# Kernel tuning notes

Measured on AMD Instinct MI355X. Metric: run time of the kernel, lower is better.

## Reference

```python
import jax, jax.numpy as jnp
import numpy as np

H = W = 128          # input_size
N = 128              # output_size[0] == output_size[1]
B = 64
LIN = (H - 2) * (W - 2)          # 15876
TRI = (N * N + N) // 2           # 8256
TI, TJ = np.triu_indices(N)
TI = jnp.asarray(TI); TJ = jnp.asarray(TJ)


def setup_inputs() -> dict:
    key = jax.random.key(0)
    ks = jax.random.split(key, 7)
    return {
        "x": jax.random.normal(ks[0], (B, 1, H, W), jnp.float32),
        "conv1_w": jax.random.normal(ks[1], (4, 1, 3, 3), jnp.float32) * 0.1,
        "conv1_b": jax.random.normal(ks[2], (4,), jnp.float32) * 0.1,
        "conv2_w": jax.random.normal(ks[3], (1, 4, 1, 1), jnp.float32) * 0.1,
        "conv2_b": jax.random.normal(ks[4], (1,), jnp.float32) * 0.1,
        "out_w": jax.random.normal(ks[5], (TRI, LIN), jnp.float32) * (1.0 / np.sqrt(LIN)),
        "out_b": jax.random.normal(ks[6], (TRI,), jnp.float32) * 0.01,
    }


def reference(x, conv1_w, conv1_b, conv2_w, conv2_b, out_w, out_b):
    dn = ('NCHW', 'OIHW', 'NCHW')
    # conv1 (1->4, 3x3, VALID) + relu
    h = jax.lax.conv_general_dilated(x, conv1_w, (1, 1), 'VALID', dimension_numbers=dn)
    h = jax.nn.relu(h + conv1_b[None, :, None, None])
    # conv2 (4->1, 1x1)
    h = jax.lax.conv_general_dilated(h, conv2_w, (1, 1), 'VALID', dimension_numbers=dn)
    h = h + conv2_b[None, :, None, None]
    # flatten -> linear
    h = h.reshape(x.shape[0], -1)                       # [B, LIN]
    v = h @ out_w.T + out_b                             # [B, TRI]
    # vectorized symmetric triu scatter (replaces per-sample Python loop)
    y = jnp.zeros((x.shape[0], N, N), v.dtype)
    y = y.at[:, TI, TJ].set(v).at[:, TJ, TI].set(v)
    return y[:, None, :, :]                             # [B, 1, N, N]
```

## Files before the change

### kernel.cpp

```cpp
#include <hip/hip_runtime.h>
#include <hip/hip_bf16.h>

#define H_IN   128
#define W_IN   128
#define B_SZ   64
#define CONV_O 126
#define K_DIM  15876
#define N_TRI  8256
#define N_OUT  128
#define BK     32
#define BN     32
#define NSTEPS 497
#define HPAD   15904
#define KSPLIT 8

typedef short  short8  __attribute__((ext_vector_type(8)));
typedef float  floatx4 __attribute__((ext_vector_type(4)));

__device__ inline short f2bf(float f) {
    union { __hip_bfloat16 h; short s; } u;
    u.h = __float2bfloat16(f);
    return u.s;
}

__global__ __launch_bounds__(256) void conv_kernel(
    const float* __restrict__ x,
    const float* __restrict__ w1,
    const float* __restrict__ b1,
    const float* __restrict__ w2,
    const float* __restrict__ b2,
    unsigned short* __restrict__ h)
{
    int t = blockIdx.x * 256 + threadIdx.x;
    int b = t / HPAD;
    int p = t - b * HPAD;
    float val = 0.f;
    if (p < K_DIM) {
        int oy = p / CONV_O;
        int ox = p - oy * CONV_O;
        const float* xb = x + b * (H_IN * W_IN) + oy * W_IN + ox;
        float xin[9];
#pragma unroll
        for (int dy = 0; dy < 3; ++dy)
#pragma unroll
            for (int dx = 0; dx < 3; ++dx)
                xin[dy * 3 + dx] = xb[dy * W_IN + dx];
        float acc = b2[0];
#pragma unroll
        for (int c = 0; c < 4; ++c) {
            float s = b1[c];
#pragma unroll
            for (int q = 0; q < 9; ++q) s = fmaf(w1[c * 9 + q], xin[q], s);
            s = fmaxf(s, 0.f);
            acc = fmaf(w2[c], s, acc);
        }
        val = acc;
    }
    h[t] = (unsigned short)f2bf(val);
}

__global__ __launch_bounds__(256, 4) void gemm_kernel(
    const unsigned short* __restrict__ h,
    const float* __restrict__ w,
    float* __restrict__ v)
{
    __shared__ __align__(16) short As[64 * 40];
    __shared__ __align__(16) short Bs[32 * 40];

    const int n0    = blockIdx.x * BN;
    const int split = blockIdx.y;
    const int s0 = (NSTEPS * split) / KSPLIT;
    const int s1 = (NSTEPS * (split + 1)) / KSPLIT;

    const int t    = threadIdx.x;
    const int lane = t & 63;
    const int wv   = t >> 6;
    const int quad = lane >> 4;
    const int l16  = lane & 15;

    const int arow = t >> 2, acol = (t & 3) * 8;
    const int brow = t >> 3, bcol = (t & 7) * 4;

    const int mh = (wv >> 1) * 32;
    const int nw = (wv & 1) * 16;

    const int aoff0 = (mh + l16) * 40 + quad * 8;
    const int aoff1 = (mh + 16 + l16) * 40 + quad * 8;
    const int boff  = (nw + l16) * 40 + quad * 8;

    floatx4 acc0 = {0.f, 0.f, 0.f, 0.f};
    floatx4 acc1 = {0.f, 0.f, 0.f, 0.f};

    for (int s = s0; s < s1; ++s) {
        const int k0 = s * BK;

        __syncthreads();
        {
            int4 av = *(const int4*)(h + (size_t)arow * HPAD + k0 + acol);
            *(int4*)(As + arow * 40 + acol) = av;
        }
        {
            const float* wp = w + (size_t)(n0 + brow) * K_DIM + k0 + bcol;
            float4 bv;
            if (k0 + BK <= K_DIM) {
                bv = *(const float4*)wp;
            } else {
                bv.x = (k0 + bcol + 0 < K_DIM) ? wp[0] : 0.f;
                bv.y = (k0 + bcol + 1 < K_DIM) ? wp[1] : 0.f;
                bv.z = (k0 + bcol + 2 < K_DIM) ? wp[2] : 0.f;
                bv.w = (k0 + bcol + 3 < K_DIM) ? wp[3] : 0.f;
            }
            short4 bs = make_short4(f2bf(bv.x), f2bf(bv.y), f2bf(bv.z), f2bf(bv.w));
            *(short4*)(Bs + brow * 40 + bcol) = bs;
        }
        __syncthreads();

        short8 af0 = *(const short8*)(As + aoff0);
        short8 af1 = *(const short8*)(As + aoff1);
        short8 bf  = *(const short8*)(Bs + boff);
        acc0 = __builtin_amdgcn_mfma_f32_16x16x32_bf16(af0, bf, acc0, 0, 0, 0);
        acc1 = __builtin_amdgcn_mfma_f32_16x16x32_bf16(af1, bf, acc1, 0, 0, 0);
    }

    const int n = n0 + nw + l16;
#pragma unroll
    for (int r = 0; r < 4; ++r) {
        int m0 = mh + quad * 4 + r;
        atomicAdd(&v[(size_t)m0 * N_TRI + n], acc0[r]);
        atomicAdd(&v[(size_t)(m0 + 16) * N_TRI + n], acc1[r]);
    }
}

__global__ __launch_bounds__(256) void scatter_kernel(
    const float* __restrict__ v,
    const float* __restrict__ out_b,
    float* __restrict__ y)
{
    int t = blockIdx.x * 256 + threadIdx.x;
    int b  = t >> 14;
    int ij = t & 16383;
    int i = ij >> 7, j = ij & 127;
    int ii = min(i, j), jj = max(i, j);
    int tri = ii * N_OUT - ((ii * (ii - 1)) >> 1) + (jj - ii);
    y[t] = v[(size_t)b * N_TRI + tri] + out_b[tri];
}

extern "C" void kernel_launch(void* const* d_in, const int* in_sizes, int n_in,
                              void* d_out, int out_size, void* d_ws, size_t ws_size,
                              hipStream_t stream) {
    const float* x   = (const float*)d_in[0];
    const float* c1w = (const float*)d_in[1];
    const float* c1b = (const float*)d_in[2];
    const float* c2w = (const float*)d_in[3];
    const float* c2b = (const float*)d_in[4];
    const float* ow  = (const float*)d_in[5];
    const float* ob  = (const float*)d_in[6];
    float* y = (float*)d_out;

    unsigned short* h = (unsigned short*)d_ws;
    float* v = (float*)((char*)d_ws + (size_t)B_SZ * HPAD * 2);

    hipMemsetAsync(v, 0, (size_t)B_SZ * N_TRI * sizeof(float), stream);

    conv_kernel<<<(B_SZ * HPAD) / 256, 256, 0, stream>>>(x, c1w, c1b, c2w, c2b, h);
    gemm_kernel<<<dim3(N_TRI / BN, KSPLIT), 256, 0, stream>>>(h, ow, v);
    scatter_kernel<<<(B_SZ * N_OUT * N_OUT) / 256, 256, 0, stream>>>(v, ob, y);
}
```

Measured before the change: 807.7 us.

## Swizzle activations into MFMA fragment layout and widen GEMM N tile

The conv kernel now writes its bf16 output in a k8-major, fragment-friendly layout, so the GEMM loads A fragments straight from global memory and no longer stages A through LDS. The N tile grows from 32 to 64 with four MFMAs per step, and the K split rises from 8 to 16 for more blocks. Each thread also loads its 8 weights before the barrier. The aim is to cut LDS traffic and per-step overhead and to overlap the weight loads better, at the cost of more atomic adds and repeated global reads of A across blocks.

```diff
diff --git a/kernel.cpp b/kernel.cpp
--- a/kernel.cpp
+++ b/kernel.cpp
@@ -9,10 +9,10 @@
 #define N_TRI  8256
 #define N_OUT  128
 #define BK     32
-#define BN     32
+#define BN     64
 #define NSTEPS 497
-#define HPAD   15904
-#define KSPLIT 8
+#define K8     1988
+#define KSPLIT 16
 
 typedef short  short8  __attribute__((ext_vector_type(8)));
 typedef float  floatx4 __attribute__((ext_vector_type(4)));
@@ -29,16 +29,18 @@
     const float* __restrict__ b1,
     const float* __restrict__ w2,
     const float* __restrict__ b2,
-    unsigned short* __restrict__ h)
+    unsigned short* __restrict__ hsw)
 {
     int t = blockIdx.x * 256 + threadIdx.x;
-    int b = t / HPAD;
-    int p = t - b * HPAD;
+    int j  = t & 7;
+    int m  = (t >> 3) & 63;
+    int k8 = t >> 9;
+    int p  = k8 * 8 + j;
     float val = 0.f;
     if (p < K_DIM) {
         int oy = p / CONV_O;
         int ox = p - oy * CONV_O;
-        const float* xb = x + b * (H_IN * W_IN) + oy * W_IN + ox;
+        const float* xb = x + m * (H_IN * W_IN) + oy * W_IN + ox;
         float xin[9];
 #pragma unroll
         for (int dy = 0; dy < 3; ++dy)
@@ -56,16 +58,15 @@
         }
         val = acc;
     }
-    h[t] = (unsigned short)f2bf(val);
+    hsw[t] = (unsigned short)f2bf(val);
 }
 
 __global__ __launch_bounds__(256, 4) void gemm_kernel(
-    const unsigned short* __restrict__ h,
+    const unsigned short* __restrict__ hsw,
     const float* __restrict__ w,
     float* __restrict__ v)
 {
-    __shared__ __align__(16) short As[64 * 40];
-    __shared__ __align__(16) short Bs[32 * 40];
+    __shared__ __align__(16) short Bs[64 * 40];
 
     const int n0    = blockIdx.x * BN;
     const int split = blockIdx.y;
@@ -78,56 +79,61 @@
     const int quad = lane >> 4;
     const int l16  = lane & 15;
 
-    const int arow = t >> 2, acol = (t & 3) * 8;
-    const int brow = t >> 3, bcol = (t & 7) * 4;
+    const int mh = (wv >> 1) * 32;
+    const int nq = (wv & 1) * 32;
 
-    const int mh = (wv >> 1) * 32;
-    const int nw = (wv & 1) * 16;
+    const int brow = t >> 2;
+    const int bk   = (t & 3) * 8;
 
-    const int aoff0 = (mh + l16) * 40 + quad * 8;
-    const int aoff1 = (mh + 16 + l16) * 40 + quad * 8;
-    const int boff  = (nw + l16) * 40 + quad * 8;
+    const int boff0 = (nq + l16) * 40 + quad * 8;
+    const int boff1 = (nq + 16 + l16) * 40 + quad * 8;
 
-    floatx4 acc0 = {0.f, 0.f, 0.f, 0.f};
-    floatx4 acc1 = {0.f, 0.f, 0.f, 0.f};
+    floatx4 acc00 = {0.f,0.f,0.f,0.f}, acc01 = {0.f,0.f,0.f,0.f};
+    floatx4 acc10 = {0.f,0.f,0.f,0.f}, acc11 = {0.f,0.f,0.f,0.f};
 
     for (int s = s0; s < s1; ++s) {
         const int k0 = s * BK;
 
+        const float* wp = w + (size_t)(n0 + brow) * K_DIM + k0 + bk;
+        float bv[8];
+        if (k0 + BK <= K_DIM) {
+            float4 x0 = *(const float4*)wp;
+            float4 x1 = *(const float4*)(wp + 4);
+            bv[0]=x0.x; bv[1]=x0.y; bv[2]=x0.z; bv[3]=x0.w;
+            bv[4]=x1.x; bv[5]=x1.y; bv[6]=x1.z; bv[7]=x1.w;
+        } else {
+#pragma unroll
+            for (int q = 0; q < 8; ++q)
+                bv[q] = (k0 + bk + q < K_DIM) ? wp[q] : 0.f;
+        }
+        short8 bs;
+#pragma unroll
+        for (int q = 0; q < 8; ++q) bs[q] = f2bf(bv[q]);
+
         __syncthreads();
-        {
-            int4 av = *(const int4*)(h + (size_t)arow * HPAD + k0 + acol);
-            *(int4*)(As + arow * 40 + acol) = av;
-        }
-        {
-            const float* wp = w + (size_t)(n0 + brow) * K_DIM + k0 + bcol;
-            float4 bv;
-            if (k0 + BK <= K_DIM) {
-                bv = *(const float4*)wp;
-            } else {
-                bv.x = (k0 + bcol + 0 < K_DIM) ? wp[0] : 0.f;
-                bv.y = (k0 + bcol + 1 < K_DIM) ? wp[1] : 0.f;
-                bv.z = (k0 + bcol + 2 < K_DIM) ? wp[2] : 0.f;
-                bv.w = (k0 + bcol + 3 < K_DIM) ? wp[3] : 0.f;
-            }
-            short4 bs = make_short4(f2bf(bv.x), f2bf(bv.y), f2bf(bv.z), f2bf(bv.w));
-            *(short4*)(Bs + brow * 40 + bcol) = bs;
-        }
+        *(short8*)(Bs + brow * 40 + bk) = bs;
         __syncthreads();
 
-        short8 af0 = *(const short8*)(As + aoff0);
-        short8 af1 = *(const short8*)(As + aoff1);
-        short8 bf  = *(const short8*)(Bs + boff);
-        acc0 = __builtin_amdgcn_mfma_f32_16x16x32_bf16(af0, bf, acc0, 0, 0, 0);
-        acc1 = __builtin_amdgcn_mfma_f32_16x16x32_bf16(af1, bf, acc1, 0, 0, 0);
+        const unsigned short* ap = hsw + (size_t)(s * 4 + quad) * (64 * 8);
+        short8 a0 = *(const short8*)(ap + (mh + l16) * 8);
+        short8 a1 = *(const short8*)(ap + (mh + 16 + l16) * 8);
+        short8 b0 = *(const short8*)(Bs + boff0);
+        short8 b1 = *(const short8*)(Bs + boff1);
+
+        acc00 = __builtin_amdgcn_mfma_f32_16x16x32_bf16(a0, b0, acc00, 0, 0, 0);
+        acc01 = __builtin_amdgcn_mfma_f32_16x16x32_bf16(a0, b1, acc01, 0, 0, 0);
+        acc10 = __builtin_amdgcn_mfma_f32_16x16x32_bf16(a1, b0, acc10, 0, 0, 0);
+        acc11 = __builtin_amdgcn_mfma_f32_16x16x32_bf16(a1, b1, acc11, 0, 0, 0);
     }
 
-    const int n = n0 + nw + l16;
+    const int nc = n0 + nq + l16;
 #pragma unroll
     for (int r = 0; r < 4; ++r) {
-        int m0 = mh + quad * 4 + r;
-        atomicAdd(&v[(size_t)m0 * N_TRI + n], acc0[r]);
-        atomicAdd(&v[(size_t)(m0 + 16) * N_TRI + n], acc1[r]);
+        int m = mh + quad * 4 + r;
+        atomicAdd(&v[(size_t)m * N_TRI + nc],              acc00[r]);
+        atomicAdd(&v[(size_t)m * N_TRI + nc + 16],         acc01[r]);
+        atomicAdd(&v[(size_t)(m + 16) * N_TRI + nc],       acc10[r]);
+        atomicAdd(&v[(size_t)(m + 16) * N_TRI + nc + 16],  acc11[r]);
     }
 }
 
@@ -157,12 +163,12 @@
     const float* ob  = (const float*)d_in[6];
     float* y = (float*)d_out;
 
-    unsigned short* h = (unsigned short*)d_ws;
-    float* v = (float*)((char*)d_ws + (size_t)B_SZ * HPAD * 2);
+    unsigned short* hsw = (unsigned short*)d_ws;
+    float* v = (float*)((char*)d_ws + (size_t)K8 * 64 * 8 * 2);
 
     hipMemsetAsync(v, 0, (size_t)B_SZ * N_TRI * sizeof(float), stream);
 
-    conv_kernel<<<(B_SZ * HPAD) / 256, 256, 0, stream>>>(x, c1w, c1b, c2w, c2b, h);
-    gemm_kernel<<<dim3(N_TRI / BN, KSPLIT), 256, 0, stream>>>(h, ow, v);
+    conv_kernel<<<(K8 * 64 * 8) / 256, 256, 0, stream>>>(x, c1w, c1b, c2w, c2b, hsw);
+    gemm_kernel<<<dim3(N_TRI / BN, KSPLIT), 256, 0, stream>>>(hsw, ow, v);
     scatter_kernel<<<(B_SZ * N_OUT * N_OUT) / 256, 256, 0, stream>>>(v, ob, y);
 }
```

Measured after the change: 733.6 us. -9.2%, faster.
